# Kernel optimization log

Hardware: AMD Instinct MI355X
Metric: run time of the kernel (lower is better)

The kernel has to match this reference:

```python
import jax, jax.numpy as jnp
import numpy as np
from jax import lax

C, H, W = 256, 56, 56
KP, STRIDE = 9, 2
M_CH, D, T = 64, 128, 16
TOPK = 32
SIGMA, ALPHA, TAU, EPS = 3.0, 10.0, 10.0, 1e-6
B = 4
N = H * W
PAD = KP // 2


def _build_M_P(h, w, s):
    ys = np.arange(0, h, s)
    xs = np.arange(0, w, s)
    ny, nx = len(ys), len(xs)
    N_, K_ = h * w, ny * nx
    by, bx = np.meshgrid(np.arange(h, dtype=np.float32), np.arange(w, dtype=np.float32), indexing='ij')
    bx = bx.reshape(-1)
    by = by.reshape(-1)
    fx, fy = bx / float(s), by / float(s)
    x0 = np.floor(fx).astype(np.int64)
    y0 = np.floor(fy).astype(np.int64)
    x0c = np.clip(x0, 0, nx - 1)
    x1c = np.clip(x0 + 1, 0, nx - 1)
    y0c = np.clip(y0, 0, ny - 1)
    y1c = np.clip(y0 + 1, 0, ny - 1)
    wx = fx - x0
    wy = fy - y0
    Mm = np.zeros((N_, K_), dtype=np.float32)
    rows = np.arange(N_)
    Mm[rows, y0c * nx + x0c] += (1 - wx) * (1 - wy)
    Mm[rows, y0c * nx + x1c] += wx * (1 - wy)
    Mm[rows, y1c * nx + x0c] += (1 - wx) * wy
    Mm[rows, y1c * nx + x1c] += wx * wy
    rs = Mm.sum(1, keepdims=True)
    rs[rs == 0] = 1.0
    Mm = Mm / rs
    P = np.stack([bx, by], axis=-1).astype(np.float32)  # (N,2) (x,y)
    return Mm, P


def _forward(feature_map, A_bank, pw_w, pw_b, proj_w, proj_b, r, M, P):
    def make_grid(A):  # affine_grid, align_corners=False
        xs = (2.0 * jnp.arange(W, dtype=jnp.float32) + 1.0) / W - 1.0
        ys = (2.0 * jnp.arange(H, dtype=jnp.float32) + 1.0) / H - 1.0
        gy, gx = jnp.meshgrid(ys, xs, indexing='ij')
        base = jnp.stack([gx, gy, jnp.ones_like(gx)], axis=-1)  # (H,W,3)
        return base @ A.T  # (H,W,2) normalized (x,y)

    def grid_sample(grid):  # bilinear, border padding, align_corners=False
        ix = ((grid[..., 0] + 1.0) * W - 1.0) / 2.0
        iy = ((grid[..., 1] + 1.0) * H - 1.0) / 2.0
        x0 = jnp.floor(ix)
        y0 = jnp.floor(iy)
        wx = ix - x0
        wy = iy - y0
        x0c = jnp.clip(x0, 0, W - 1).astype(jnp.int32)
        x1c = jnp.clip(x0 + 1, 0, W - 1).astype(jnp.int32)
        y0c = jnp.clip(y0, 0, H - 1).astype(jnp.int32)
        y1c = jnp.clip(y0 + 1, 0, H - 1).astype(jnp.int32)
        fm = feature_map.reshape(B, C, H * W)
        def g(yc, xc):
            return fm[:, :, (yc * W + xc).reshape(-1)].reshape(B, C, H, W)
        return (g(y0c, x0c) * (1 - wx) * (1 - wy) + g(y0c, x1c) * wx * (1 - wy)
                + g(y1c, x0c) * (1 - wx) * wy + g(y1c, x1c) * wx * wy)

    grids = jax.vmap(make_grid)(A_bank)          # (T,H,W,2)
    warped = jax.vmap(grid_sample)(grids)        # (T,B,C,H,W)

    # unfold(k,pad,stride) -> 1x1 conv -> spatial mean  ==  zero-padded avg-pool then linear
    pm = lax.reduce_window(warped, 0.0, lax.add,
                           (1, 1, 1, KP, KP), (1, 1, 1, STRIDE, STRIDE),
                           [(0, 0), (0, 0), (0, 0), (PAD, PAD), (PAD, PAD)]) / (KP * KP)
    Tn, Bn, Cn, Kh, Kw = pm.shape
    K = Kh * Kw
    pm = pm.reshape(Tn, Bn, Cn, K).transpose(0, 1, 3, 2)  # (T,B,K,C)
    x = pm @ pw_w.T + pw_b                                 # (T,B,K,m)
    z = x @ proj_w.T + proj_b                              # (T,B,K,d)
    z = z / jnp.maximum(jnp.linalg.norm(z, axis=-1, keepdims=True), EPS)
    Z = z.transpose(1, 0, 2, 3)                            # (B,T,K,d)

    s = jnp.einsum('btkd,d->btk', Z, r)
    wgt = jax.nn.softmax(TAU * s, axis=1)[..., None]
    g_emb = jnp.sum(wgt * Z, axis=1)                       # (B,K,d)

    E = jnp.einsum('nk,bkd->bnd', M, g_emb)
    E = E / jnp.maximum(jnp.linalg.norm(E, axis=-1, keepdims=True), EPS)

    d2 = jnp.sum((P[:, None, :] - P[None, :, :]) ** 2, axis=-1)  # (N,N)
    G = 1.0 - jnp.exp(-d2 / (2.0 * SIGMA ** 2))
    Saff = jnp.einsum('bnd,bmd->bnm', E, E) * G

    vals, idx = lax.top_k(Saff, TOPK)
    bidx = jnp.arange(B)[:, None, None]
    nidx = jnp.arange(N)[None, :, None]
    S_sp = jnp.zeros_like(Saff).at[bidx, nidx, idx].set(vals)
    A0 = jax.nn.softmax(ALPHA * S_sp, axis=-1) * jax.nn.softmax(ALPHA * S_sp, axis=-2)
    return E, A0


def setup_inputs() -> dict:
    key = jax.random.key(0)
    ks = jax.random.split(key, 6)
    feature_map = jax.random.normal(ks[0], (B, C, H, W), jnp.float32)
    ident = jnp.broadcast_to(jnp.array([[1.0, 0.0, 0.0], [0.0, 1.0, 0.0]], jnp.float32), (T, 2, 3))
    A_bank = ident + 0.1 * jax.random.normal(ks[1], (T, 2, 3), jnp.float32)
    pw_w = jax.random.normal(ks[2], (M_CH, C), jnp.float32) / np.sqrt(C).astype(np.float32)
    pw_b = jnp.zeros((M_CH,), jnp.float32)
    proj_w = jax.random.normal(ks[3], (D, M_CH), jnp.float32) / np.sqrt(M_CH).astype(np.float32)
    proj_b = jnp.zeros((D,), jnp.float32)
    r = 0.01 * jax.random.normal(ks[4], (D,), jnp.float32)
    Mnp, Pnp = _build_M_P(H, W, STRIDE)
    return {'feature_map': feature_map, 'A_bank': A_bank, 'pw_w': pw_w, 'pw_b': pw_b,
            'proj_w': proj_w, 'proj_b': proj_b, 'r': r,
            'M': jnp.asarray(Mnp), 'P': jnp.asarray(Pnp)}


def reference(feature_map, A_bank, pw_w, pw_b, proj_w, proj_b, r, M, P):
    return _forward(feature_map, A_bank, pw_w, pw_b, proj_w, proj_b, r, M, P)
```

## Files before the change

### kernel.cpp

```cpp
#include <hip/hip_runtime.h>
#include <hip/hip_bf16.h>
#include <hip/hip_fp16.h>

#define Hh 56
#define Ww 56
#define Cc 256
#define Tt 16
#define Bb 4
#define Nn 3136
#define Kk 784
#define KX 28
#define Dd 128
#define Mc 64
#define NTOP 32

typedef __attribute__((ext_vector_type(8))) _Float16 f16x8;
typedef __attribute__((ext_vector_type(4))) float f32x4;

__global__ __launch_bounds__(128) void k_wc(
    const float* __restrict__ pw_w, const float* __restrict__ pw_b,
    const float* __restrict__ proj_w, const float* __restrict__ proj_b,
    float* __restrict__ wct, float* __restrict__ bc) {
  int c = blockIdx.x;
  int d = threadIdx.x;
  float acc = 0.f;
  for (int m = 0; m < Mc; ++m) acc += proj_w[d * Mc + m] * pw_w[m * Cc + c];
  wct[c * Dd + d] = acc;
  if (c == 0) {
    float bb = proj_b[d];
    for (int m = 0; m < Mc; ++m) bb += proj_w[d * Mc + m] * pw_b[m];
    bc[d] = bb;
  }
}

__global__ __launch_bounds__(256) void k_mix(
    const float* __restrict__ fm, const float* __restrict__ wct, float* __restrict__ y) {
  int blk = blockIdx.x;
  int b = blk / 112;
  int n0 = (blk % 112) * 28;
  int tid = threadIdx.x;
  int d = tid & 127;
  int ng = tid >> 7;
  __shared__ float fm_s[64 * 28];
  __shared__ float wc_s[64 * Dd];
  float acc[14];
#pragma unroll
  for (int j = 0; j < 14; ++j) acc[j] = 0.f;
  const float* fb = fm + (size_t)b * Cc * Nn;
  for (int c0 = 0; c0 < Cc; c0 += 64) {
    for (int i = tid; i < 64 * 28; i += 256) {
      int c = i / 28, kx = i - c * 28;
      fm_s[i] = fb[(size_t)(c0 + c) * Nn + n0 + kx];
    }
    for (int i = tid; i < 64 * Dd; i += 256) wc_s[i] = wct[c0 * Dd + i];
    __syncthreads();
    for (int c = 0; c < 64; ++c) {
      float w = wc_s[c * Dd + d];
#pragma unroll
      for (int j = 0; j < 14; ++j) acc[j] += fm_s[c * 28 + ng * 14 + j] * w;
    }
    __syncthreads();
  }
  float* yo = y + ((size_t)b * Dd + d) * Nn + n0 + ng * 14;
#pragma unroll
  for (int j = 0; j < 14; ++j) yo[j] = acc[j];
}

__global__ __launch_bounds__(256) void k_fused_pool(
    const float* __restrict__ y, const float* __restrict__ Abank,
    const float* __restrict__ bc, float* __restrict__ zt) {
  int idx = blockIdx.x;
  int b = idx & 3;
  int dg = (idx >> 2) & 31;
  int t = idx >> 7;
  __shared__ float wsm[3136];
  __shared__ float rowp[1568];
  int tid = threadIdx.x;
  const float* A = Abank + t * 6;
  float a00 = A[0], a01 = A[1], a02 = A[2], a10 = A[3], a11 = A[4], a12 = A[5];
  int off[13];
  float wxa[13], wya[13];
#pragma unroll
  for (int j = 0; j < 13; ++j) {
    int e = tid + 256 * j;
    if (e < 3136) {
      int h = e / 56, w = e - h * 56;
      float gx = (2.0f * w + 1.0f) / 56.0f - 1.0f;
      float gy = (2.0f * h + 1.0f) / 56.0f - 1.0f;
      float u = a00 * gx + a01 * gy + a02;
      float v = a10 * gx + a11 * gy + a12;
      float ix = ((u + 1.0f) * 56.0f - 1.0f) * 0.5f;
      float iy = ((v + 1.0f) * 56.0f - 1.0f) * 0.5f;
      float x0f = floorf(ix), y0f = floorf(iy);
      wxa[j] = ix - x0f;
      wya[j] = iy - y0f;
      int x0 = (int)x0f, y0 = (int)y0f;
      int x0c = min(max(x0, 0), 55), x1c = min(max(x0 + 1, 0), 55);
      int y0c = min(max(y0, 0), 55), y1c = min(max(y0 + 1, 0), 55);
      off[j] = (y0c * 56 + x0c) | ((x1c - x0c) << 12) | ((y1c - y0c) << 13);
    }
  }
  for (int dd = 0; dd < 4; ++dd) {
    int d = dg * 4 + dd;
    const float* fc = y + ((size_t)b * Dd + d) * Nn;
    float bias = bc[d];
#pragma unroll
    for (int j = 0; j < 13; ++j) {
      int e = tid + 256 * j;
      if (e < 3136) {
        int pk = off[j];
        int base = pk & 4095;
        int dx = (pk >> 12) & 1;
        int dyy = (pk & (1 << 13)) ? 56 : 0;
        float v00 = fc[base], v01 = fc[base + dx];
        float v10 = fc[base + dyy], v11 = fc[base + dyy + dx];
        float wx = wxa[j], wy = wya[j];
        float top = v00 + wx * (v01 - v00);
        float bot = v10 + wx * (v11 - v10);
        wsm[e] = top + wy * (bot - top);
      }
    }
    __syncthreads();
    for (int e = tid; e < 1568; e += 256) {
      int h = e / 28, kx = e - h * 28;
      int xs = 2 * kx - 4;
      int lo = max(xs, 0), hi = min(xs + 8, 55);
      float s = 0.f;
      const float* wr = wsm + h * 56;
      for (int x = lo; x <= hi; ++x) s += wr[x];
      rowp[e] = s;
    }
    __syncthreads();
    float* zo = zt + ((size_t)(t * Bb + b) * Dd + d) * Kk;
    for (int e = tid; e < 784; e += 256) {
      int ky = e / 28, kx = e - ky * 28;
      int ys = 2 * ky - 4;
      int lo = max(ys, 0), hi = min(ys + 8, 55);
      float s = 0.f;
      for (int h = lo; h <= hi; ++h) s += rowp[h * 28 + kx];
      zo[e] = s * (1.0f / 81.0f) + bias;
    }
    __syncthreads();
  }
}

__global__ __launch_bounds__(256) void k_znorm(
    const float* __restrict__ zt, const float* __restrict__ r,
    float* __restrict__ z, float* __restrict__ s_arr) {
  int tb = blockIdx.x / 14;
  int k0 = (blockIdx.x % 14) * 56;
  int tid = threadIdx.x;
  __shared__ float ls[56 * 129];
  const float* zb = zt + (size_t)tb * Dd * Kk + k0;
  for (int i = tid; i < Dd * 56; i += 256) {
    int d = i / 56, kk = i - d * 56;
    ls[kk * 129 + d] = zb[(size_t)d * Kk + kk];
  }
  int lane = tid & 63;
  int wv = tid >> 6;
  float r0 = r[lane], r1 = r[lane + 64];
  __syncthreads();
  for (int p = 0; p < 14; ++p) {
    int k = p * 4 + wv;
    float z0 = ls[k * 129 + lane];
    float z1 = ls[k * 129 + 64 + lane];
    float ss = z0 * z0 + z1 * z1;
    for (int off = 32; off; off >>= 1) ss += __shfl_xor(ss, off);
    float inv = 1.0f / fmaxf(sqrtf(ss), 1e-6f);
    z0 *= inv; z1 *= inv;
    float* zr = z + ((size_t)tb * Kk + k0 + k) * Dd;
    zr[lane] = z0;
    zr[lane + 64] = z1;
    float sd = z0 * r0 + z1 * r1;
    for (int off = 32; off; off >>= 1) sd += __shfl_xor(sd, off);
    if (lane == 0) s_arr[(size_t)tb * Kk + k0 + k] = sd;
  }
}

__global__ __launch_bounds__(128) void k_gemb(
    const float* __restrict__ z, const float* __restrict__ s_arr, float* __restrict__ g) {
  int blk = blockIdx.x;
  int b = blk / Kk, k = blk % Kk;
  int d = threadIdx.x;
  float sv[Tt];
  float mx = -3.4e38f;
#pragma unroll
  for (int t = 0; t < Tt; ++t) {
    sv[t] = s_arr[(t * Bb + b) * Kk + k];
    mx = fmaxf(mx, sv[t]);
  }
  float sum = 0.f;
#pragma unroll
  for (int t = 0; t < Tt; ++t) {
    sv[t] = expf(10.0f * (sv[t] - mx));
    sum += sv[t];
  }
  float isum = 1.0f / sum;
  float acc = 0.f;
#pragma unroll
  for (int t = 0; t < Tt; ++t)
    acc += sv[t] * isum * z[((size_t)(t * Bb + b) * Kk + k) * Dd + d];
  g[((size_t)b * Kk + k) * Dd + d] = acc;
}

__global__ __launch_bounds__(64) void k_E(
    const float* __restrict__ Mmat, const float* __restrict__ g,
    float* __restrict__ E, _Float16* __restrict__ E16) {
  int row = blockIdx.x;
  int b = row / Nn, n = row % Nn;
  int y = n / Ww, x = n % Ww;
  int x0 = x >> 1, y0 = y >> 1;
  int x1 = min(x0 + 1, 27), y1 = min(y0 + 1, 27);
  bool hx = (x1 != x0), hy = (y1 != y0);
  int k00 = y0 * 28 + x0, k01 = y0 * 28 + x1, k10 = y1 * 28 + x0, k11 = y1 * 28 + x1;
  const float* Mr = Mmat + (size_t)n * Kk;
  float m00 = Mr[k00];
  float m01 = hx ? Mr[k01] : 0.f;
  float m10 = hy ? Mr[k10] : 0.f;
  float m11 = (hx && hy) ? Mr[k11] : 0.f;
  const float* gb = g + (size_t)b * Kk * Dd;
  int lane = threadIdx.x;
  int l2 = lane + 64;
  float a0 = m00 * gb[k00 * Dd + lane] + m01 * gb[k01 * Dd + lane] +
             m10 * gb[k10 * Dd + lane] + m11 * gb[k11 * Dd + lane];
  float a1 = m00 * gb[k00 * Dd + l2] + m01 * gb[k01 * Dd + l2] +
             m10 * gb[k10 * Dd + l2] + m11 * gb[k11 * Dd + l2];
  float ss = a0 * a0 + a1 * a1;
  for (int off = 32; off; off >>= 1) ss += __shfl_xor(ss, off);
  float inv = 1.0f / fmaxf(sqrtf(ss), 1e-6f);
  float e0 = a0 * inv, e1 = a1 * inv;
  E[(size_t)row * Dd + lane] = e0;
  E[(size_t)row * Dd + l2] = e1;
  E16[(size_t)row * Dd + lane] = (_Float16)e0;
  E16[(size_t)row * Dd + l2] = (_Float16)e1;
}

__global__ __launch_bounds__(256) void k_saff(
    const _Float16* __restrict__ E16, __half* __restrict__ S) {
  int blk = blockIdx.x;
  int b = blk / 1225;
  int rem = blk % 1225;
  int ti0 = (int)((sqrtf(8.f * rem + 1.f) - 1.f) * 0.5f);
  while ((ti0 + 1) * (ti0 + 2) / 2 <= rem) ++ti0;
  while (ti0 * (ti0 + 1) / 2 > rem) --ti0;
  int tj0 = rem - ti0 * (ti0 + 1) / 2;
  int i0 = ti0 * 64, j0 = tj0 * 64;
  int wave = threadIdx.x >> 6, lane = threadIdx.x & 63;
  int wr = wave >> 1, wc = wave & 1;
  int lr = lane & 15, lk = lane >> 4;
  int ibase = i0 + wr * 32;
  int jbase = j0 + wc * 32;
  const _Float16* Eb = E16 + (size_t)b * Nn * Dd;
  f32x4 acc00 = {0.f, 0.f, 0.f, 0.f};
  f32x4 acc01 = acc00, acc10 = acc00, acc11 = acc00;
#pragma unroll
  for (int ks = 0; ks < 4; ++ks) {
    int ko = ks * 32 + lk * 8;
    f16x8 a0 = *reinterpret_cast<const f16x8*>(Eb + (size_t)(ibase + lr) * Dd + ko);
    f16x8 a1 = *reinterpret_cast<const f16x8*>(Eb + (size_t)(ibase + 16 + lr) * Dd + ko);
    f16x8 b0 = *reinterpret_cast<const f16x8*>(Eb + (size_t)(jbase + lr) * Dd + ko);
    f16x8 b1 = *reinterpret_cast<const f16x8*>(Eb + (size_t)(jbase + 16 + lr) * Dd + ko);
    acc00 = __builtin_amdgcn_mfma_f32_16x16x32_f16(a0, b0, acc00, 0, 0, 0);
    acc01 = __builtin_amdgcn_mfma_f32_16x16x32_f16(a0, b1, acc01, 0, 0, 0);
    acc10 = __builtin_amdgcn_mfma_f32_16x16x32_f16(a1, b0, acc10, 0, 0, 0);
    acc11 = __builtin_amdgcn_mfma_f32_16x16x32_f16(a1, b1, acc11, 0, 0, 0);
  }
  size_t ob = (size_t)b * Nn * Nn;
  int gj[2];
  float xj[2], yj[2];
#pragma unroll
  for (int tj = 0; tj < 2; ++tj) {
    gj[tj] = jbase + tj * 16 + lr;
    int yv = gj[tj] / 56;
    yj[tj] = (float)yv;
    xj[tj] = (float)(gj[tj] - yv * 56);
  }
  bool mirror = (i0 != j0);
#pragma unroll
  for (int ti = 0; ti < 2; ++ti) {
#pragma unroll
    for (int q = 0; q < 4; ++q) {
      int gi = ibase + ti * 16 + lk * 4 + q;
      int yiv = gi / 56;
      float yi = (float)yiv;
      float xi = (float)(gi - yiv * 56);
#pragma unroll
      for (int tj = 0; tj < 2; ++tj) {
        float a;
        if (ti == 0 && tj == 0) a = acc00[q];
        else if (ti == 0 && tj == 1) a = acc01[q];
        else if (ti == 1 && tj == 0) a = acc10[q];
        else a = acc11[q];
        float dx = xi - xj[tj];
        float dy = yi - yj[tj];
        float gg = 1.0f - __expf(-(dx * dx + dy * dy) * (1.0f / 18.0f));
        __half hv = __float2half(a * gg);
        S[ob + (size_t)gi * Nn + gj[tj]] = hv;
        if (mirror) S[ob + (size_t)gj[tj] * Nn + gi] = hv;
      }
    }
  }
}

__global__ __launch_bounds__(256) void k_topk(
    const __half* __restrict__ S16, const float* __restrict__ E,
    const float* __restrict__ P, float* __restrict__ topv, int* __restrict__ topi,
    float* __restrict__ dr, float* __restrict__ dc) {
  int row = blockIdx.x;
  int b = row / Nn, irow = row % Nn;
  int tid = threadIdx.x;
  const unsigned* Sr = reinterpret_cast<const unsigned*>(S16 + (size_t)row * Nn);
  __shared__ unsigned hist[256 * 8];
  __shared__ unsigned scan_s[256];
  __shared__ unsigned bcast[2];
  __shared__ unsigned sel_eq, sel_slot;
  __shared__ int sel_idx[NTOP];
  __shared__ float drow_s;
  unsigned pk[7];
#pragma unroll
  for (int j = 0; j < 7; ++j) {
    int c2 = tid + 256 * j;
    unsigned u = (c2 < Nn / 2) ? Sr[c2] : 0u;
    unsigned h0 = u & 0xFFFFu, h1 = u >> 16;
    unsigned k0 = h0 ^ ((h0 & 0x8000u) ? 0xFFFFu : 0x8000u);
    unsigned k1 = h1 ^ ((h1 & 0x8000u) ? 0xFFFFu : 0x8000u);
    if (c2 >= Nn / 2) { k0 = 0u; k1 = 0u; }
    pk[j] = k0 | (k1 << 16);
  }
  if (tid == 0) { sel_eq = 0; sel_slot = 0; drow_s = 0.f; }
  unsigned prefix = 0;
  unsigned k = NTOP;
  for (int pass = 0; pass < 2; ++pass) {
    int shift = 8 - 8 * pass;
    unsigned pmask = pass ? 0xFF00u : 0u;
#pragma unroll
    for (int i = 0; i < 8; ++i) hist[tid * 8 + i] = 0;
    __syncthreads();
#pragma unroll
    for (int j = 0; j < 7; ++j) {
      unsigned k0 = pk[j] & 0xFFFFu, k1 = pk[j] >> 16;
      if ((k0 & pmask) == (prefix & pmask))
        atomicAdd(&hist[((k0 >> shift) & 255u) * 8 + (tid & 7)], 1u);
      if ((k1 & pmask) == (prefix & pmask))
        atomicAdd(&hist[((k1 >> shift) & 255u) * 8 + (tid & 7)], 1u);
    }
    __syncthreads();
    unsigned cnt = 0;
#pragma unroll
    for (int i = 0; i < 8; ++i) cnt += hist[tid * 8 + i];
    unsigned run = cnt;
    scan_s[tid] = run;
    for (int st = 1; st < 256; st <<= 1) {
      __syncthreads();
      unsigned add = (tid + st < 256) ? scan_s[tid + st] : 0u;
      __syncthreads();
      run += add;
      scan_s[tid] = run;
    }
    unsigned incl = run;
    unsigned excl = incl - cnt;
    if (excl < k && k <= incl) {
      bcast[0] = prefix | ((unsigned)tid << shift);
      bcast[1] = k - excl;
    }
    __syncthreads();
    prefix = bcast[0];
    k = bcast[1];
    __syncthreads();
  }
  unsigned T = prefix;
#pragma unroll
  for (int j = 0; j < 7; ++j) {
    int c2 = tid + 256 * j;
    if (c2 < Nn / 2) {
      unsigned k0 = pk[j] & 0xFFFFu, k1 = pk[j] >> 16;
      bool take0 = (k0 > T) || (k0 == T && atomicAdd(&sel_eq, 1u) < k);
      if (take0) { unsigned slot = atomicAdd(&sel_slot, 1u); sel_idx[slot] = 2 * c2; }
      bool take1 = (k1 > T) || (k1 == T && atomicAdd(&sel_eq, 1u) < k);
      if (take1) { unsigned slot = atomicAdd(&sel_slot, 1u); sel_idx[slot] = 2 * c2 + 1; }
    }
  }
  __syncthreads();
  int sel = tid >> 3, part = tid & 7;
  int col = sel_idx[sel];
  const float* Ei = E + ((size_t)b * Nn + irow) * Dd;
  const float* Ej = E + ((size_t)b * Nn + col) * Dd;
  float v = 0.f;
#pragma unroll
  for (int d0 = 0; d0 < 16; ++d0) {
    int d = part * 16 + d0;
    v += Ei[d] * Ej[d];
  }
  v += __shfl_xor(v, 1);
  v += __shfl_xor(v, 2);
  v += __shfl_xor(v, 4);
  if (part == 0) {
    float dx = P[irow * 2] - P[col * 2];
    float dy = P[irow * 2 + 1] - P[col * 2 + 1];
    float gg = 1.0f - __expf(-(dx * dx + dy * dy) * (1.0f / 18.0f));
    v *= gg;
    topv[(size_t)row * NTOP + sel] = v;
    topi[(size_t)row * NTOP + sel] = col;
    float e = __expf(10.f * v);
    atomicAdd(&dc[b * Nn + col], e - 1.f);
    atomicAdd(&drow_s, e);
  }
  __syncthreads();
  if (tid == 0) dr[row] = (float)(Nn - NTOP) + drow_s;
}

__global__ void k_dcinit(float* __restrict__ dc) {
  int i = blockIdx.x * 256 + threadIdx.x;
  if (i < Bb * Nn) dc[i] = (float)Nn;
}

__global__ void k_inv(float* __restrict__ dr, float* __restrict__ dc) {
  int i = blockIdx.x * 256 + threadIdx.x;
  if (i < Bb * Nn) {
    dr[i] = 1.0f / dr[i];
    dc[i] = 1.0f / dc[i];
  }
}

__global__ __launch_bounds__(256) void k_basefix(
    const float* __restrict__ invdr, const float* __restrict__ invdc,
    const float* __restrict__ topv, const int* __restrict__ topi,
    float* __restrict__ A0) {
  int row = blockIdx.x;
  int b = row / Nn;
  float idr = invdr[row];
  const float4* dc4 = reinterpret_cast<const float4*>(invdc + b * Nn);
  float4* out4 = reinterpret_cast<float4*>(A0 + (size_t)row * Nn);
  for (int j = threadIdx.x; j < Nn / 4; j += 256) {
    float4 c = dc4[j];
    float4 o = {idr * c.x, idr * c.y, idr * c.z, idr * c.w};
    out4[j] = o;
  }
  __syncthreads();
  if (threadIdx.x < NTOP) {
    int gidx = row * NTOP + threadIdx.x;
    int col = topi[gidx];
    float e = __expf(10.f * topv[gidx]);
    A0[(size_t)row * Nn + col] = e * e * idr * invdc[b * Nn + col];
  }
}

extern "C" void kernel_launch(void* const* d_in, const int* in_sizes, int n_in,
                              void* d_out, int out_size, void* d_ws, size_t ws_size,
                              hipStream_t stream) {
  const float* fm     = (const float*)d_in[0];
  const float* Abank  = (const float*)d_in[1];
  const float* pw_w   = (const float*)d_in[2];
  const float* pw_b   = (const float*)d_in[3];
  const float* proj_w = (const float*)d_in[4];
  const float* proj_b = (const float*)d_in[5];
  const float* r      = (const float*)d_in[6];
  const float* Mmat   = (const float*)d_in[7];
  const float* P      = (const float*)d_in[8];
  float* out = (float*)d_out;
  float* E  = out;
  float* A0 = out + (size_t)Bb * Nn * Dd;
  __half* S16 = (__half*)A0;

  float* ws = (float*)d_ws;
  float* y     = ws;
  float* zt    = ws + 1605632;
  float* z     = ws + 8028160;
  float* wct   = ws + 14450688;
  float* bcv   = ws + 14483456;
  float* s_arr = ws + 14483584;
  float* g     = ws + 14533760;
  float* topv  = ws + 14935168;
  int*   topi  = (int*)(ws + 15336576);
  float* dr    = ws + 15737984;
  float* dc    = ws + 15750528;
  _Float16* E16 = (_Float16*)(ws + 15763072);

  hipLaunchKernelGGL(k_wc, dim3(Cc), dim3(128), 0, stream, pw_w, pw_b, proj_w, proj_b, wct, bcv);
  hipLaunchKernelGGL(k_mix, dim3(448), dim3(256), 0, stream, fm, wct, y);
  hipLaunchKernelGGL(k_fused_pool, dim3(2048), dim3(256), 0, stream, y, Abank, bcv, zt);
  hipLaunchKernelGGL(k_znorm, dim3(64 * 14), dim3(256), 0, stream, zt, r, z, s_arr);
  hipLaunchKernelGGL(k_gemb, dim3(Bb * Kk), dim3(128), 0, stream, z, s_arr, g);
  hipLaunchKernelGGL(k_E, dim3(Bb * Nn), dim3(64), 0, stream, Mmat, g, E, E16);
  hipLaunchKernelGGL(k_saff, dim3(Bb * 1225), dim3(256), 0, stream, E16, S16);
  hipLaunchKernelGGL(k_dcinit, dim3(49), dim3(256), 0, stream, dc);
  hipLaunchKernelGGL(k_topk, dim3(Bb * Nn), dim3(256), 0, stream, S16, E, P, topv, topi, dr, dc);
  hipLaunchKernelGGL(k_inv, dim3(49), dim3(256), 0, stream, dr, dc);
  hipLaunchKernelGGL(k_basefix, dim3(Bb * Nn), dim3(256), 0, stream, dr, dc, topv, topi, A0);
}
```

Before: 489.8 us.

## Interleave channel pairs in y for float2 pooling; stage mirrored S tile in LDS

The projection kernel now writes y with pairs of output channels interleaved, so the pooling kernel can gather float2 values and process two channels per bilinear lookup. This halves the number of scattered gathers and the loop iterations per channel, at the cost of doubling the shared memory for wsm and rowp. Separately, the similarity kernel now writes the mirrored (transposed) half of S through a padded LDS tile with coalesced 32-bit stores. This replaces the strided 2-byte scattered writes, adding one barrier.

```diff
diff --git a/kernel.cpp b/kernel.cpp
--- a/kernel.cpp
+++ b/kernel.cpp
@@ -61,20 +61,21 @@
     }
     __syncthreads();
   }
-  float* yo = y + ((size_t)b * Dd + d) * Nn + n0 + ng * 14;
-#pragma unroll
-  for (int j = 0; j < 14; ++j) yo[j] = acc[j];
+  size_t base = (((size_t)b * 64 + (d >> 1)) * Nn + n0 + ng * 14) * 2 + (d & 1);
+#pragma unroll
+  for (int j = 0; j < 14; ++j) y[base + 2 * j] = acc[j];
 }
 
 __global__ __launch_bounds__(256) void k_fused_pool(
-    const float* __restrict__ y, const float* __restrict__ Abank,
+    const float* __restrict__ yraw, const float* __restrict__ Abank,
     const float* __restrict__ bc, float* __restrict__ zt) {
+  const float2* y2 = reinterpret_cast<const float2*>(yraw);
   int idx = blockIdx.x;
   int b = idx & 3;
-  int dg = (idx >> 2) & 31;
+  int pg = (idx >> 2) & 31;
   int t = idx >> 7;
-  __shared__ float wsm[3136];
-  __shared__ float rowp[1568];
+  __shared__ float2 wsm[3136];
+  __shared__ float2 rowp[1568];
   int tid = threadIdx.x;
   const float* A = Abank + t * 6;
   float a00 = A[0], a01 = A[1], a02 = A[2], a10 = A[3], a11 = A[4], a12 = A[5];
@@ -100,10 +101,10 @@
       off[j] = (y0c * 56 + x0c) | ((x1c - x0c) << 12) | ((y1c - y0c) << 13);
     }
   }
-  for (int dd = 0; dd < 4; ++dd) {
-    int d = dg * 4 + dd;
-    const float* fc = y + ((size_t)b * Dd + d) * Nn;
-    float bias = bc[d];
+  for (int pp = 0; pp < 2; ++pp) {
+    int dp = pg * 2 + pp;
+    const float2* fc = y2 + ((size_t)b * 64 + dp) * Nn;
+    float b0 = bc[dp * 2], b1 = bc[dp * 2 + 1];
 #pragma unroll
     for (int j = 0; j < 13; ++j) {
       int e = tid + 256 * j;
@@ -112,12 +113,17 @@
         int base = pk & 4095;
         int dx = (pk >> 12) & 1;
         int dyy = (pk & (1 << 13)) ? 56 : 0;
-        float v00 = fc[base], v01 = fc[base + dx];
-        float v10 = fc[base + dyy], v11 = fc[base + dyy + dx];
+        float2 v00 = fc[base], v01 = fc[base + dx];
+        float2 v10 = fc[base + dyy], v11 = fc[base + dyy + dx];
         float wx = wxa[j], wy = wya[j];
-        float top = v00 + wx * (v01 - v00);
-        float bot = v10 + wx * (v11 - v10);
-        wsm[e] = top + wy * (bot - top);
+        float tx = v00.x + wx * (v01.x - v00.x);
+        float bx = v10.x + wx * (v11.x - v10.x);
+        float ty = v00.y + wx * (v01.y - v00.y);
+        float by = v10.y + wx * (v11.y - v10.y);
+        float2 o;
+        o.x = tx + wy * (bx - tx);
+        o.y = ty + wy * (by - ty);
+        wsm[e] = o;
       }
     }
     __syncthreads();
@@ -125,20 +131,23 @@
       int h = e / 28, kx = e - h * 28;
       int xs = 2 * kx - 4;
       int lo = max(xs, 0), hi = min(xs + 8, 55);
-      float s = 0.f;
-      const float* wr = wsm + h * 56;
-      for (int x = lo; x <= hi; ++x) s += wr[x];
-      rowp[e] = s;
-    }
-    __syncthreads();
-    float* zo = zt + ((size_t)(t * Bb + b) * Dd + d) * Kk;
+      float sx = 0.f, sy = 0.f;
+      const float2* wr = wsm + h * 56;
+      for (int x = lo; x <= hi; ++x) { float2 v = wr[x]; sx += v.x; sy += v.y; }
+      float2 o; o.x = sx; o.y = sy;
+      rowp[e] = o;
+    }
+    __syncthreads();
+    float* zo0 = zt + ((size_t)(t * Bb + b) * Dd + dp * 2) * Kk;
+    float* zo1 = zo0 + Kk;
     for (int e = tid; e < 784; e += 256) {
       int ky = e / 28, kx = e - ky * 28;
       int ys = 2 * ky - 4;
       int lo = max(ys, 0), hi = min(ys + 8, 55);
-      float s = 0.f;
-      for (int h = lo; h <= hi; ++h) s += rowp[h * 28 + kx];
-      zo[e] = s * (1.0f / 81.0f) + bias;
+      float sx = 0.f, sy = 0.f;
+      for (int h = lo; h <= hi; ++h) { float2 rv = rowp[h * 28 + kx]; sx += rv.x; sy += rv.y; }
+      zo0[e] = sx * (1.0f / 81.0f) + b0;
+      zo1[e] = sy * (1.0f / 81.0f) + b1;
     }
     __syncthreads();
   }
@@ -251,6 +260,7 @@
   int ibase = i0 + wr * 32;
   int jbase = j0 + wc * 32;
   const _Float16* Eb = E16 + (size_t)b * Nn * Dd;
+  __shared__ __half tile[64][66];
   f32x4 acc00 = {0.f, 0.f, 0.f, 0.f};
   f32x4 acc01 = acc00, acc10 = acc00, acc11 = acc00;
 #pragma unroll
@@ -280,7 +290,8 @@
   for (int ti = 0; ti < 2; ++ti) {
 #pragma unroll
     for (int q = 0; q < 4; ++q) {
-      int gi = ibase + ti * 16 + lk * 4 + q;
+      int iloc = wr * 32 + ti * 16 + lk * 4 + q;
+      int gi = i0 + iloc;
       int yiv = gi / 56;
       float yi = (float)yiv;
       float xi = (float)(gi - yiv * 56);
@@ -296,8 +307,17 @@
         float gg = 1.0f - __expf(-(dx * dx + dy * dy) * (1.0f / 18.0f));
         __half hv = __float2half(a * gg);
         S[ob + (size_t)gi * Nn + gj[tj]] = hv;
-        if (mirror) S[ob + (size_t)gj[tj] * Nn + gi] = hv;
+        int jloc = wc * 32 + tj * 16 + lr;
+        tile[jloc][iloc] = hv;
       }
+    }
+  }
+  if (mirror) {
+    __syncthreads();
+    for (int e = threadIdx.x; e < 64 * 32; e += 256) {
+      int row = e >> 5, c2 = e & 31;
+      unsigned v = *reinterpret_cast<const unsigned*>(&tile[row][c2 * 2]);
+      *reinterpret_cast<unsigned*>(&S[ob + (size_t)(j0 + row) * Nn + i0 + c2 * 2]) = v;
     }
   }
 }
```

Result: faster. 436.4 us (-10.9%).
